# Performance work log

Hardware: AMD Instinct MI355X
Metric: run time of the kernel (lower is better)

## Reference

```python
import jax, jax.numpy as jnp
import numpy as np

N_NODES = 100000
N_EDGES = 3200000
N_FEAT = 128


def setup_inputs() -> dict:
    key = jax.random.key(0)
    ks = jax.random.split(key, 8)
    x = jax.random.normal(ks[0], (N_NODES, N_FEAT), dtype=jnp.float32)
    edge_index = jax.random.randint(ks[1], (2, N_EDGES), 0, N_NODES, dtype=jnp.int64)

    def glorot(k, fan_in, fan_out):
        s = (6.0 / (fan_in + fan_out)) ** 0.5
        return jax.random.uniform(k, (fan_in, fan_out), jnp.float32, -s, s)

    return {
        "x": x,
        "edge_index": edge_index,
        "W1": glorot(ks[2], N_FEAT, 64), "b1": jnp.zeros((64,), jnp.float32),
        "W2": glorot(ks[3], 64, 32),     "b2": jnp.zeros((32,), jnp.float32),
        "W3": glorot(ks[4], 32, 2),      "b3": jnp.zeros((2,), jnp.float32),
    }


def _gcn_norm(edge_index, num_nodes):
    # Add self loops, then symmetric normalization D^{-1/2} (A+I) D^{-1/2}
    loop = jnp.arange(num_nodes, dtype=edge_index.dtype)
    src = jnp.concatenate([edge_index[0], loop])
    dst = jnp.concatenate([edge_index[1], loop])
    deg = jax.ops.segment_sum(jnp.ones_like(dst, dtype=jnp.float32), dst,
                              num_segments=num_nodes)
    dinv = jnp.where(deg > 0, jax.lax.rsqrt(deg), 0.0)
    norm = dinv[src] * dinv[dst]  # [E + N]
    return src, dst, norm


def _gcn_conv(h, W, b, src, dst, norm, num_nodes):
    h = h @ W  # small dense GEMM
    msg = h[src] * norm[:, None]  # gather + scale
    out = jax.ops.segment_sum(msg, dst, num_segments=num_nodes)  # scatter-add
    return out + b


def reference(x, edge_index, W1, b1, W2, b2, W3, b3):
    n = x.shape[0]
    src, dst, norm = _gcn_norm(edge_index, n)
    h = jax.nn.relu(_gcn_conv(x, W1, b1, src, dst, norm, n))
    # dropout(p=0.5) is identity in eval mode
    h = jax.nn.relu(_gcn_conv(h, W2, b2, src, dst, norm, n))
    h = _gcn_conv(h, W3, b3, src, dst, norm, n)
    return jax.nn.log_softmax(h, axis=1)
```

## Files before the change

### kernel.cpp

```cpp
#include <hip/hip_runtime.h>
#include <math.h>

#define EPB 4096
#define CAP 10240

typedef __attribute__((ext_vector_type(8))) short bf16x8;
typedef __attribute__((ext_vector_type(4))) float f32x4;
typedef __attribute__((ext_vector_type(2))) float f32x2;


__device__ inline unsigned short f2b(float f) {
  union { float f; unsigned u; } c; c.f = f;
  unsigned r = c.u + 0x7fff + ((c.u >> 16) & 1);
  return (unsigned short)(r >> 16);
}


__global__ __launch_bounds__(256) void k_bscan2(const int* __restrict__ cnts, int* __restrict__ bbase,
                                                int* __restrict__ rowptr, int E, int N, int NBKT) {
  __shared__ int a[512], c[512];
  int tid = threadIdx.x;
  int v0 = (tid < NBKT) ? cnts[tid] : 0;
  int v1 = (tid + 256 < NBKT) ? cnts[tid + 256] : 0;
  a[tid] = v0; a[tid + 256] = v1;
  __syncthreads();
  int* pin = a; int* pout = c;
  for (int st = 1; st < 512; st <<= 1) {
    pout[tid]       = pin[tid]       + ((tid >= st)       ? pin[tid - st]       : 0);
    pout[tid + 256] = pin[tid + 256] + ((tid + 256 >= st) ? pin[tid + 256 - st] : 0);
    __syncthreads();
    int* t = pin; pin = pout; pout = t;
  }
  if (tid < NBKT)       bbase[tid] = pin[tid] - v0;
  if (tid + 256 < NBKT) bbase[tid + 256] = pin[tid + 256] - v1;
  if (tid == 0) { bbase[NBKT] = E; rowptr[N] = E; }
}


__global__ __launch_bounds__(512) void k_bucket_scatter(const int* __restrict__ src, const int* __restrict__ dst,
                                                        int* __restrict__ gcur, unsigned* __restrict__ tmp,
                                                        int E, int NBKT) {
  __shared__ int hist[512], base[512], loff[512];
  __shared__ int sa[512], sc[512];
  __shared__ unsigned stage[EPB];
  __shared__ unsigned short bkt16[EPB];
  int tid = threadIdx.x;
  int ebeg = blockIdx.x * EPB;
  int eend = min(E, ebeg + EPB);
  hist[tid] = 0;
  __syncthreads();
  int e0 = ebeg + tid * 8;
  int nE = eend - e0; if (nE < 0) nE = 0; if (nE > 8) nE = 8;
  int d[8], s[8], rk[8];
  if (nE == 8) {
#pragma unroll
    for (int q = 0; q < 2; ++q) {
      int4 dv = *(const int4*)(dst + e0 + q * 4);
      int4 sv = *(const int4*)(src + e0 + q * 4);
      d[q * 4 + 0] = dv.x; d[q * 4 + 1] = dv.y; d[q * 4 + 2] = dv.z; d[q * 4 + 3] = dv.w;
      s[q * 4 + 0] = sv.x; s[q * 4 + 1] = sv.y; s[q * 4 + 2] = sv.z; s[q * 4 + 3] = sv.w;
    }
  } else {
#pragma unroll
    for (int k = 0; k < 8; ++k) {
      if (k < nE) { d[k] = dst[e0 + k]; s[k] = src[e0 + k]; } else { d[k] = 0; s[k] = 0; }
    }
  }
#pragma unroll
  for (int k = 0; k < 8; ++k) rk[k] = (k < nE) ? atomicAdd(&hist[d[k] >> 8], 1) : 0;
  __syncthreads();
  int hc = hist[tid];
  sa[tid] = hc;
  base[tid] = (tid < NBKT && hc) ? atomicAdd(&gcur[tid], hc) : 0;
  __syncthreads();
  int* pin = sa; int* pout = sc;
  for (int st = 1; st < 512; st <<= 1) {
    pout[tid] = pin[tid] + ((tid >= st) ? pin[tid - st] : 0);
    __syncthreads();
    int* t = pin; pin = pout; pout = t;
  }
  loff[tid] = pin[tid] - hc;
  __syncthreads();
#pragma unroll
  for (int k = 0; k < 8; ++k) if (k < nE) {
    int bkt = d[k] >> 8;
    int pos = loff[bkt] + rk[k];
    stage[pos] = ((unsigned)s[k] << 8) | (unsigned)(d[k] & 255);
    bkt16[pos] = (unsigned short)bkt;
  }
  __syncthreads();
  int cnt = eend - ebeg;
  for (int k = tid; k < cnt; k += 512) {
    int b = bkt16[k];
    tmp[(size_t)b * CAP + base[b] + (k - loff[b])] = stage[k];
  }
}


__global__ __launch_bounds__(512) void k_bucket_build(const unsigned* __restrict__ tmp, const int* __restrict__ cnts,
                                                      const int* __restrict__ bbase, int* __restrict__ csr,
                                                      int* __restrict__ rowptr, float* __restrict__ dinv, int N) {
  int b = blockIdx.x;
  int tid = threadIdx.x;
  int node0 = b << 8;
  int nn = min(256, N - node0);
  int cnt = cnts[b];
  int gbeg = bbase[b];
  const unsigned* tb = tmp + (size_t)b * CAP;
  __shared__ int h[256], off[256], cur[256];
  __shared__ unsigned short rk[CAP];
  __shared__ int stage[CAP];
  if (tid < 256) h[tid] = 0;
  __syncthreads();
  bool fast = (cnt <= CAP);
  if (fast) {
    for (int e = tid; e < cnt; e += 512) {
      unsigned p = tb[e];
      rk[e] = (unsigned short)atomicAdd(&h[p & 255], 1);
    }
  } else {
    for (int e = tid; e < cnt; e += 512) atomicAdd(&h[tb[e] & 255], 1);
  }
  __syncthreads();
  int deg = 0;
  if (tid < 256) { deg = h[tid]; off[tid] = deg; }
  __syncthreads();
  for (int st = 1; st < 256; st <<= 1) {
    int t = 0;
    if (tid < 256 && tid >= st) t = off[tid - st];
    __syncthreads();
    if (tid < 256) off[tid] += t;
    __syncthreads();
  }
  if (tid < 256) {
    int excl = off[tid] - deg;
    cur[tid] = excl;
    if (tid < nn) {
      rowptr[node0 + tid] = gbeg + excl;
      dinv[node0 + tid] = rsqrtf((float)(deg + 1));
    }
  }
  __syncthreads();
  if (fast) {
    for (int e = tid; e < cnt; e += 512) {
      unsigned p = tb[e];
      stage[cur[p & 255] + (int)rk[e]] = (int)(p >> 8);
    }
    __syncthreads();
    for (int k = tid; k < cnt; k += 512) csr[gbeg + k] = stage[k];
  } else {
    for (int e = tid; e < cnt; e += 512) {
      unsigned p = tb[e];
      int pos = atomicAdd(&cur[p & 255], 1);
      csr[gbeg + pos] = (int)(p >> 8);
    }
  }
}


template <int F_IN, int F_OUT>
__global__ __launch_bounds__(256) void k_gemm_mfma(const float* __restrict__ x, const float* __restrict__ W,
                                                   const float* __restrict__ dinv, unsigned short* __restrict__ g,
                                                   int N, int NT) {
  constexpr int NKS = F_IN / 32;
  constexpr int NCT = F_OUT / 16;
  int tid = threadIdx.x;
  int w = tid >> 6, lane = tid & 63;
  int lo = lane & 15, hi = lane >> 4;

  union U8 { bf16x8 v; unsigned u[4]; };
  U8 bf[NCT][NKS];
#pragma unroll
  for (int ct = 0; ct < NCT; ++ct)
#pragma unroll
    for (int ks = 0; ks < NKS; ++ks) {
      const float* wp = W + (size_t)(ks * 32 + hi * 8) * F_OUT + ct * 16 + lo;
      float f[8];
#pragma unroll
      for (int j = 0; j < 8; ++j) f[j] = wp[(size_t)j * F_OUT];
#pragma unroll
      for (int j = 0; j < 4; ++j)
        asm("v_cvt_pk_bf16_f32 %0, %1, %2" : "=v"(bf[ct][ks].u[j]) : "v"(f[2 * j]), "v"(f[2 * j + 1]));
    }

  for (int t = blockIdx.x * 4 + w; t < NT; t += gridDim.x * 4) {
    int row0 = t << 4;
    f32x4 acc[NCT];
#pragma unroll
    for (int ct = 0; ct < NCT; ++ct) acc[ct] = (f32x4){0.f, 0.f, 0.f, 0.f};
    int rl = row0 + lo; if (rl >= N) rl = N - 1;
    const float* xrow = x + (size_t)rl * F_IN;
#pragma unroll
    for (int ks = 0; ks < NKS; ++ks) {
      const float* xp = xrow + ks * 32 + hi * 8;
      float4 a0 = *(const float4*)xp;
      float4 a1 = *(const float4*)(xp + 4);
      U8 af;
      asm("v_cvt_pk_bf16_f32 %0, %1, %2" : "=v"(af.u[0]) : "v"(a0.x), "v"(a0.y));
      asm("v_cvt_pk_bf16_f32 %0, %1, %2" : "=v"(af.u[1]) : "v"(a0.z), "v"(a0.w));
      asm("v_cvt_pk_bf16_f32 %0, %1, %2" : "=v"(af.u[2]) : "v"(a1.x), "v"(a1.y));
      asm("v_cvt_pk_bf16_f32 %0, %1, %2" : "=v"(af.u[3]) : "v"(a1.z), "v"(a1.w));
#pragma unroll
      for (int ct = 0; ct < NCT; ++ct)
        acc[ct] = __builtin_amdgcn_mfma_f32_16x16x32_bf16(af.v, bf[ct][ks].v, acc[ct], 0, 0, 0);
    }
    float dvv[4];
    if (row0 + 16 <= N) {
      float4 d4 = *(const float4*)(dinv + row0 + (hi << 2));
      dvv[0] = d4.x; dvv[1] = d4.y; dvv[2] = d4.z; dvv[3] = d4.w;
    } else {
#pragma unroll
      for (int j = 0; j < 4; ++j) { int r = row0 + (hi << 2) + j; dvv[j] = dinv[r < N ? r : N - 1]; }
    }
#pragma unroll
    for (int ct = 0; ct < NCT; ++ct) {
#pragma unroll
      for (int j = 0; j < 4; ++j) {
        int row = row0 + (hi << 2) + j;
        if (row < N) g[(size_t)row * F_OUT + ct * 16 + lo] = f2b(dvv[j] * acc[ct][j]);
      }
    }
  }
}


#define ACC2(vv) acc0 += __uint_as_float((vv) << 16); acc1 += __uint_as_float((vv) & 0xffff0000u)

template <int FOUT, bool RELU>
__global__ __launch_bounds__(256) void k_agg_full(const unsigned short* __restrict__ g,
                                                  const int* __restrict__ rowptr, const int* __restrict__ csr,
                                                  const float* __restrict__ dinv, const float* __restrict__ bias,
                                                  float* __restrict__ out, int N) {
  constexpr int LSH = (FOUT == 64) ? 5 : 4;
  constexpr int RSH = (FOUT == 64) ? 7 : 6;
  int t = blockIdx.x * 256 + threadIdx.x;
  int grp = t >> LSH;
  if (grp >= N) return;
  unsigned subB = ((unsigned)t & ((1u << LSH) - 1u)) << 2;
  const char* gb = (const char*)g;
  auto gat = [&](int sid) -> unsigned {
    return *(const unsigned*)(gb + ((((unsigned)sid) << RSH) + subB));
  };
  unsigned u = gat(grp);
  float acc0 = __uint_as_float(u << 16);
  float acc1 = __uint_as_float(u & 0xffff0000u);
  int beg = rowptr[grp], end = rowptr[grp + 1];
  int j = beg;
  for (; j < end && (j & 3); ++j) {
    unsigned v = gat(csr[j]); ACC2(v);
  }
  for (; j + 16 <= end; j += 16) {
    int4 sA = *(const int4*)(csr + j);
    int4 sB = *(const int4*)(csr + j + 4);
    int4 sC = *(const int4*)(csr + j + 8);
    int4 sD = *(const int4*)(csr + j + 12);
    unsigned v0 = gat(sA.x), v1 = gat(sA.y), v2 = gat(sA.z), v3 = gat(sA.w);
    unsigned v4 = gat(sB.x), v5 = gat(sB.y), v6 = gat(sB.z), v7 = gat(sB.w);
    unsigned v8 = gat(sC.x), v9 = gat(sC.y), vA = gat(sC.z), vB = gat(sC.w);
    unsigned vC = gat(sD.x), vD = gat(sD.y), vE = gat(sD.z), vF = gat(sD.w);
    ACC2(v0); ACC2(v1); ACC2(v2); ACC2(v3);
    ACC2(v4); ACC2(v5); ACC2(v6); ACC2(v7);
    ACC2(v8); ACC2(v9); ACC2(vA); ACC2(vB);
    ACC2(vC); ACC2(vD); ACC2(vE); ACC2(vF);
  }
  if (j + 8 <= end) {
    int4 sA = *(const int4*)(csr + j);
    int4 sB = *(const int4*)(csr + j + 4);
    unsigned v0 = gat(sA.x), v1 = gat(sA.y), v2 = gat(sA.z), v3 = gat(sA.w);
    unsigned v4 = gat(sB.x), v5 = gat(sB.y), v6 = gat(sB.z), v7 = gat(sB.w);
    ACC2(v0); ACC2(v1); ACC2(v2); ACC2(v3);
    ACC2(v4); ACC2(v5); ACC2(v6); ACC2(v7);
    j += 8;
  }
  if (j + 4 <= end) {
    int4 sA = *(const int4*)(csr + j);
    unsigned v0 = gat(sA.x), v1 = gat(sA.y), v2 = gat(sA.z), v3 = gat(sA.w);
    ACC2(v0); ACC2(v1); ACC2(v2); ACC2(v3);
    j += 4;
  }
  for (; j < end; ++j) {
    unsigned v = gat(csr[j]); ACC2(v);
  }
  float dv = dinv[grp];
  int fg = (int)(subB >> 1);
  float r0 = fmaf(dv, acc0, bias[fg]);
  float r1 = fmaf(dv, acc1, bias[fg + 1]);
  if (RELU) { r0 = fmaxf(r0, 0.f); r1 = fmaxf(r1, 0.f); }
  *(float2*)(out + (size_t)grp * FOUT + fg) = make_float2(r0, r1);
}


__global__ __launch_bounds__(256) void k_agg2f(const unsigned short* __restrict__ g,
                                               const int* __restrict__ rowptr, const int* __restrict__ csr,
                                               const float* __restrict__ dinv, const float* __restrict__ b2,
                                               const float* __restrict__ W3, unsigned* __restrict__ g2, int N) {
  int t = blockIdx.x * 256 + threadIdx.x;
  int grp = t >> 4;
  if (grp >= N) return;
  unsigned subB = ((unsigned)t & 15u) << 2;
  const char* gb = (const char*)g;
  auto gat = [&](int sid) -> unsigned {
    return *(const unsigned*)(gb + ((((unsigned)sid) << 6) + subB));
  };
  unsigned u = gat(grp);
  float acc0 = __uint_as_float(u << 16);
  float acc1 = __uint_as_float(u & 0xffff0000u);
  int beg = rowptr[grp], end = rowptr[grp + 1];
  int j = beg;
  for (; j < end && (j & 3); ++j) {
    unsigned v = gat(csr[j]); ACC2(v);
  }
  for (; j + 16 <= end; j += 16) {
    int4 sA = *(const int4*)(csr + j);
    int4 sB = *(const int4*)(csr + j + 4);
    int4 sC = *(const int4*)(csr + j + 8);
    int4 sD = *(const int4*)(csr + j + 12);
    unsigned v0 = gat(sA.x), v1 = gat(sA.y), v2 = gat(sA.z), v3 = gat(sA.w);
    unsigned v4 = gat(sB.x), v5 = gat(sB.y), v6 = gat(sB.z), v7 = gat(sB.w);
    unsigned v8 = gat(sC.x), v9 = gat(sC.y), vA = gat(sC.z), vB = gat(sC.w);
    unsigned vC = gat(sD.x), vD = gat(sD.y), vE = gat(sD.z), vF = gat(sD.w);
    ACC2(v0); ACC2(v1); ACC2(v2); ACC2(v3);
    ACC2(v4); ACC2(v5); ACC2(v6); ACC2(v7);
    ACC2(v8); ACC2(v9); ACC2(vA); ACC2(vB);
    ACC2(vC); ACC2(vD); ACC2(vE); ACC2(vF);
  }
  if (j + 8 <= end) {
    int4 sA = *(const int4*)(csr + j);
    int4 sB = *(const int4*)(csr + j + 4);
    unsigned v0 = gat(sA.x), v1 = gat(sA.y), v2 = gat(sA.z), v3 = gat(sA.w);
    unsigned v4 = gat(sB.x), v5 = gat(sB.y), v6 = gat(sB.z), v7 = gat(sB.w);
    ACC2(v0); ACC2(v1); ACC2(v2); ACC2(v3);
    ACC2(v4); ACC2(v5); ACC2(v6); ACC2(v7);
    j += 8;
  }
  if (j + 4 <= end) {
    int4 sA = *(const int4*)(csr + j);
    unsigned v0 = gat(sA.x), v1 = gat(sA.y), v2 = gat(sA.z), v3 = gat(sA.w);
    ACC2(v0); ACC2(v1); ACC2(v2); ACC2(v3);
    j += 4;
  }
  for (; j < end; ++j) {
    unsigned v = gat(csr[j]); ACC2(v);
  }
  float dv = dinv[grp];
  int fg = (int)(subB >> 1);
  float r0 = fmaxf(fmaf(dv, acc0, b2[fg]), 0.f);
  float r1 = fmaxf(fmaf(dv, acc1, b2[fg + 1]), 0.f);
  float4 wv = *(const float4*)(W3 + subB);
  float p0 = r0 * wv.x + r1 * wv.z;
  float p1 = r0 * wv.y + r1 * wv.w;
#pragma unroll
  for (int m = 1; m < 16; m <<= 1) { p0 += __shfl_xor(p0, m); p1 += __shfl_xor(p1, m); }
  if ((t & 15) == 0) {
    unsigned uo = (unsigned)f2b(dv * p0) | ((unsigned)f2b(dv * p1) << 16);
    g2[grp] = uo;
  }
}


__global__ __launch_bounds__(256) void k_final(const unsigned* __restrict__ g2, const int* __restrict__ rowptr,
                                               const int* __restrict__ csr, const float* __restrict__ dinv,
                                               const float* __restrict__ bias, float* __restrict__ out, int N) {
  int i = blockIdx.x * 256 + threadIdx.x;
  if (i >= N) return;
  const char* gb = (const char*)g2;
  unsigned s = *(const unsigned*)(gb + (((unsigned)i) << 2));
  float a0 = __uint_as_float(s << 16), a1 = __uint_as_float(s & 0xffff0000u);
  int beg = rowptr[i], end = rowptr[i + 1];
  int j = beg;
  for (; j < end && (j & 3); ++j) {
    unsigned p = *(const unsigned*)(gb + (((unsigned)csr[j]) << 2));
    a0 += __uint_as_float(p << 16);
    a1 += __uint_as_float(p & 0xffff0000u);
  }
  for (; j + 4 <= end; j += 4) {
    int4 ss = *(const int4*)(csr + j);
    unsigned p0 = *(const unsigned*)(gb + (((unsigned)ss.x) << 2));
    unsigned p1 = *(const unsigned*)(gb + (((unsigned)ss.y) << 2));
    unsigned p2 = *(const unsigned*)(gb + (((unsigned)ss.z) << 2));
    unsigned p3 = *(const unsigned*)(gb + (((unsigned)ss.w) << 2));
    a0 += __uint_as_float(p0 << 16); a1 += __uint_as_float(p0 & 0xffff0000u);
    a0 += __uint_as_float(p1 << 16); a1 += __uint_as_float(p1 & 0xffff0000u);
    a0 += __uint_as_float(p2 << 16); a1 += __uint_as_float(p2 & 0xffff0000u);
    a0 += __uint_as_float(p3 << 16); a1 += __uint_as_float(p3 & 0xffff0000u);
  }
  for (; j < end; ++j) {
    unsigned p = *(const unsigned*)(gb + (((unsigned)csr[j]) << 2));
    a0 += __uint_as_float(p << 16);
    a1 += __uint_as_float(p & 0xffff0000u);
  }
  float dv = dinv[i];
  float v0 = fmaf(dv, a0, bias[0]);
  float v1 = fmaf(dv, a1, bias[1]);
  float m = fmaxf(v0, v1);
  float lse = m + logf(expf(v0 - m) + expf(v1 - m));
  f32x2 o; o.x = v0 - lse; o.y = v1 - lse;
  __builtin_nontemporal_store(o, (f32x2*)(out + 2 * (size_t)i));
}


extern "C" void kernel_launch(void* const* d_in, const int* in_sizes, int n_in,
                              void* d_out, int out_size, void* d_ws, size_t ws_size,
                              hipStream_t stream) {
  const float* x  = (const float*)d_in[0];
  const int*   ei = (const int*)d_in[1];
  const float* W1 = (const float*)d_in[2];
  const float* b1 = (const float*)d_in[3];
  const float* W2 = (const float*)d_in[4];
  const float* b2 = (const float*)d_in[5];
  const float* W3 = (const float*)d_in[6];
  const float* b3 = (const float*)d_in[7];
  float* out = (float*)d_out;

  int N = in_sizes[0] / 128;
  int E = in_sizes[1] / 2;
  const int* src = ei;
  const int* dst = ei + E;
  int NBKT = (N + 255) >> 8;
  int NT = (N + 15) / 16;

  char* w = (char*)d_ws;
  size_t off = 0;
  auto carve = [&](size_t bytes) -> char* {
    char* p = w + off;
    off = (off + bytes + 255) & ~(size_t)255;
    return p;
  };
  float* dinv   = (float*)carve((size_t)N * 4);
  int*   rowptr = (int*)carve((size_t)(N + 1) * 4);
  int*   bbase  = (int*)carve(2048 + 4);
  int*   gcur   = (int*)carve(2048);
  int*   csr    = (int*)carve((size_t)E * 4);
  size_t gsz = (size_t)N * 64 * 2;
  size_t capb = (size_t)NBKT * CAP * 4;
  if (capb > gsz) gsz = capb;
  unsigned short* gbuf = (unsigned short*)carve(gsz);
  float* hbuf   = (float*)carve((size_t)N * 64 * 4);
  unsigned* tmp = (unsigned*)gbuf;
  (void)ws_size; (void)n_in; (void)out_size;

  (void)hipMemsetAsync(gcur, 0, 2048, stream);
  k_bucket_scatter<<<(E + EPB - 1) / EPB, 512, 0, stream>>>(src, dst, gcur, tmp, E, NBKT);
  k_bscan2<<<1, 256, 0, stream>>>(gcur, bbase, rowptr, E, N, NBKT);
  k_bucket_build<<<NBKT, 512, 0, stream>>>(tmp, gcur, bbase, csr, rowptr, dinv, N);

  k_gemm_mfma<128, 64><<<782, 256, 0, stream>>>(x, W1, dinv, gbuf, N, NT);
  k_agg_full<64, true><<<(unsigned)(((long long)N * 32 + 255) / 256), 256, 0, stream>>>(gbuf, rowptr, csr, dinv, b1, hbuf, N);
  k_gemm_mfma<64, 32><<<782, 256, 0, stream>>>(hbuf, W2, dinv, gbuf, N, NT);
  unsigned* g2 = (unsigned*)hbuf;
  k_agg2f<<<(unsigned)(((long long)N * 16 + 255) / 256), 256, 0, stream>>>(gbuf, rowptr, csr, dinv, b2, W3, g2, N);
  k_final<<<(unsigned)((N + 255) / 256), 256, 0, stream>>>(g2, rowptr, csr, dinv, b3, out, N);
}
```

Before: 201.5 us.

## Store layer-1 activations in bf16, fold bucket scan into build, split accumulators

The layer-1 aggregation now writes ReLU output as bf16 instead of fp32, and a new bf16-input MFMA GEMM reads it. This halves the intermediate traffic between aggregation and the second GEMM. The separate single-block bucket prefix-scan kernel is removed: each build block redoes the 512-entry scan in shared memory, which saves a launch but repeats the work in every block. Both aggregation kernels also use two interleaved accumulator pairs to shorten the dependent add chains, and the extra bf16 rounding slightly changes the numerics.

Measured after the change: 199.5 us. About the same (-1.0%).

```diff
diff --git a/kernel.cpp b/kernel.cpp
--- a/kernel.cpp
+++ b/kernel.cpp
@@ -13,27 +13,6 @@
   union { float f; unsigned u; } c; c.f = f;
   unsigned r = c.u + 0x7fff + ((c.u >> 16) & 1);
   return (unsigned short)(r >> 16);
-}
-
-
-__global__ __launch_bounds__(256) void k_bscan2(const int* __restrict__ cnts, int* __restrict__ bbase,
-                                                int* __restrict__ rowptr, int E, int N, int NBKT) {
-  __shared__ int a[512], c[512];
-  int tid = threadIdx.x;
-  int v0 = (tid < NBKT) ? cnts[tid] : 0;
-  int v1 = (tid + 256 < NBKT) ? cnts[tid + 256] : 0;
-  a[tid] = v0; a[tid + 256] = v1;
-  __syncthreads();
-  int* pin = a; int* pout = c;
-  for (int st = 1; st < 512; st <<= 1) {
-    pout[tid]       = pin[tid]       + ((tid >= st)       ? pin[tid - st]       : 0);
-    pout[tid + 256] = pin[tid + 256] + ((tid + 256 >= st) ? pin[tid + 256 - st] : 0);
-    __syncthreads();
-    int* t = pin; pin = pout; pout = t;
-  }
-  if (tid < NBKT)       bbase[tid] = pin[tid] - v0;
-  if (tid + 256 < NBKT) bbase[tid + 256] = pin[tid + 256] - v1;
-  if (tid == 0) { bbase[NBKT] = E; rowptr[N] = E; }
 }
 
 
@@ -98,20 +77,33 @@
 
 
 __global__ __launch_bounds__(512) void k_bucket_build(const unsigned* __restrict__ tmp, const int* __restrict__ cnts,
-                                                      const int* __restrict__ bbase, int* __restrict__ csr,
-                                                      int* __restrict__ rowptr, float* __restrict__ dinv, int N) {
+                                                      int* __restrict__ csr, int* __restrict__ rowptr,
+                                                      float* __restrict__ dinv, int E, int N, int NBKT) {
   int b = blockIdx.x;
   int tid = threadIdx.x;
   int node0 = b << 8;
   int nn = min(256, N - node0);
-  int cnt = cnts[b];
-  int gbeg = bbase[b];
-  const unsigned* tb = tmp + (size_t)b * CAP;
+  __shared__ int sa[512], sc[512];
   __shared__ int h[256], off[256], cur[256];
   __shared__ unsigned short rk[CAP];
   __shared__ int stage[CAP];
+  __shared__ int gbeg_sh;
+  int v = (tid < NBKT) ? cnts[tid] : 0;
+  sa[tid] = v;
   if (tid < 256) h[tid] = 0;
   __syncthreads();
+  int* pin = sa; int* pout = sc;
+  for (int st = 1; st < 512; st <<= 1) {
+    pout[tid] = pin[tid] + ((tid >= st) ? pin[tid - st] : 0);
+    __syncthreads();
+    int* t = pin; pin = pout; pout = t;
+  }
+  if (tid == b) gbeg_sh = pin[tid] - v;
+  if (b == 0 && tid == 0) rowptr[N] = E;
+  __syncthreads();
+  int cnt = cnts[b];
+  int gbeg = gbeg_sh;
+  const unsigned* tb = tmp + (size_t)b * CAP;
   bool fast = (cnt <= CAP);
   if (fast) {
     for (int e = tid; e < cnt; e += 512) {
@@ -224,30 +216,88 @@
 }
 
 
-#define ACC2(vv) acc0 += __uint_as_float((vv) << 16); acc1 += __uint_as_float((vv) & 0xffff0000u)
-
-template <int FOUT, bool RELU>
-__global__ __launch_bounds__(256) void k_agg_full(const unsigned short* __restrict__ g,
-                                                  const int* __restrict__ rowptr, const int* __restrict__ csr,
-                                                  const float* __restrict__ dinv, const float* __restrict__ bias,
-                                                  float* __restrict__ out, int N) {
-  constexpr int LSH = (FOUT == 64) ? 5 : 4;
-  constexpr int RSH = (FOUT == 64) ? 7 : 6;
+template <int F_IN, int F_OUT>
+__global__ __launch_bounds__(256) void k_gemm_mfma_b(const unsigned short* __restrict__ xb, const float* __restrict__ W,
+                                                     const float* __restrict__ dinv, unsigned short* __restrict__ g,
+                                                     int N, int NT) {
+  constexpr int NKS = F_IN / 32;
+  constexpr int NCT = F_OUT / 16;
+  int tid = threadIdx.x;
+  int w = tid >> 6, lane = tid & 63;
+  int lo = lane & 15, hi = lane >> 4;
+
+  union U8 { bf16x8 v; unsigned u[4]; };
+  U8 bf[NCT][NKS];
+#pragma unroll
+  for (int ct = 0; ct < NCT; ++ct)
+#pragma unroll
+    for (int ks = 0; ks < NKS; ++ks) {
+      const float* wp = W + (size_t)(ks * 32 + hi * 8) * F_OUT + ct * 16 + lo;
+      float f[8];
+#pragma unroll
+      for (int j = 0; j < 8; ++j) f[j] = wp[(size_t)j * F_OUT];
+#pragma unroll
+      for (int j = 0; j < 4; ++j)
+        asm("v_cvt_pk_bf16_f32 %0, %1, %2" : "=v"(bf[ct][ks].u[j]) : "v"(f[2 * j]), "v"(f[2 * j + 1]));
+    }
+
+  for (int t = blockIdx.x * 4 + w; t < NT; t += gridDim.x * 4) {
+    int row0 = t << 4;
+    f32x4 acc[NCT];
+#pragma unroll
+    for (int ct = 0; ct < NCT; ++ct) acc[ct] = (f32x4){0.f, 0.f, 0.f, 0.f};
+    int rl = row0 + lo; if (rl >= N) rl = N - 1;
+    const unsigned short* xrow = xb + (size_t)rl * F_IN;
+#pragma unroll
+    for (int ks = 0; ks < NKS; ++ks) {
+      bf16x8 av = *(const bf16x8*)(xrow + ks * 32 + hi * 8);
+#pragma unroll
+      for (int ct = 0; ct < NCT; ++ct)
+        acc[ct] = __builtin_amdgcn_mfma_f32_16x16x32_bf16(av, bf[ct][ks].v, acc[ct], 0, 0, 0);
+    }
+    float dvv[4];
+    if (row0 + 16 <= N) {
+      float4 d4 = *(const float4*)(dinv + row0 + (hi << 2));
+      dvv[0] = d4.x; dvv[1] = d4.y; dvv[2] = d4.z; dvv[3] = d4.w;
+    } else {
+#pragma unroll
+      for (int j = 0; j < 4; ++j) { int r = row0 + (hi << 2) + j; dvv[j] = dinv[r < N ? r : N - 1]; }
+    }
+#pragma unroll
+    for (int ct = 0; ct < NCT; ++ct) {
+#pragma unroll
+      for (int j = 0; j < 4; ++j) {
+        int row = row0 + (hi << 2) + j;
+        if (row < N) g[(size_t)row * F_OUT + ct * 16 + lo] = f2b(dvv[j] * acc[ct][j]);
+      }
+    }
+  }
+}
+
+
+#define ACCa(vv) a0a += __uint_as_float((vv) << 16); a1a += __uint_as_float((vv) & 0xffff0000u)
+#define ACCb(vv) a0b += __uint_as_float((vv) << 16); a1b += __uint_as_float((vv) & 0xffff0000u)
+
+__global__ __launch_bounds__(256) void k_agg1(const unsigned short* __restrict__ g,
+                                              const int* __restrict__ rowptr, const int* __restrict__ csr,
+                                              const float* __restrict__ dinv, const float* __restrict__ bias,
+                                              unsigned short* __restrict__ h1b, int N) {
   int t = blockIdx.x * 256 + threadIdx.x;
-  int grp = t >> LSH;
+  int grp = t >> 5;
   if (grp >= N) return;
-  unsigned subB = ((unsigned)t & ((1u << LSH) - 1u)) << 2;
+  unsigned subB = ((unsigned)t & 31u) << 2;
   const char* gb = (const char*)g;
   auto gat = [&](int sid) -> unsigned {
-    return *(const unsigned*)(gb + ((((unsigned)sid) << RSH) + subB));
+    return *(const unsigned*)(gb + ((((unsigned)sid) << 7) + subB));
   };
   unsigned u = gat(grp);
-  float acc0 = __uint_as_float(u << 16);
-  float acc1 = __uint_as_float(u & 0xffff0000u);
+  float a0a = __uint_as_float(u << 16);
+  float a1a = __uint_as_float(u & 0xffff0000u);
+  float a0b = 0.f, a1b = 0.f;
   int beg = rowptr[grp], end = rowptr[grp + 1];
   int j = beg;
   for (; j < end && (j & 3); ++j) {
-    unsigned v = gat(csr[j]); ACC2(v);
+    unsigned v = gat(csr[j]); ACCa(v);
   }
   for (; j + 16 <= end; j += 16) {
     int4 sA = *(const int4*)(csr + j);
@@ -258,35 +308,36 @@
     unsigned v4 = gat(sB.x), v5 = gat(sB.y), v6 = gat(sB.z), v7 = gat(sB.w);
     unsigned v8 = gat(sC.x), v9 = gat(sC.y), vA = gat(sC.z), vB = gat(sC.w);
     unsigned vC = gat(sD.x), vD = gat(sD.y), vE = gat(sD.z), vF = gat(sD.w);
-    ACC2(v0); ACC2(v1); ACC2(v2); ACC2(v3);
-    ACC2(v4); ACC2(v5); ACC2(v6); ACC2(v7);
-    ACC2(v8); ACC2(v9); ACC2(vA); ACC2(vB);
-    ACC2(vC); ACC2(vD); ACC2(vE); ACC2(vF);
+    ACCa(v0); ACCb(v1); ACCa(v2); ACCb(v3);
+    ACCa(v4); ACCb(v5); ACCa(v6); ACCb(v7);
+    ACCa(v8); ACCb(v9); ACCa(vA); ACCb(vB);
+    ACCa(vC); ACCb(vD); ACCa(vE); ACCb(vF);
   }
   if (j + 8 <= end) {
     int4 sA = *(const int4*)(csr + j);
     int4 sB = *(const int4*)(csr + j + 4);
     unsigned v0 = gat(sA.x), v1 = gat(sA.y), v2 = gat(sA.z), v3 = gat(sA.w);
     unsigned v4 = gat(sB.x), v5 = gat(sB.y), v6 = gat(sB.z), v7 = gat(sB.w);
-    ACC2(v0); ACC2(v1); ACC2(v2); ACC2(v3);
-    ACC2(v4); ACC2(v5); ACC2(v6); ACC2(v7);
+    ACCa(v0); ACCb(v1); ACCa(v2); ACCb(v3);
+    ACCa(v4); ACCb(v5); ACCa(v6); ACCb(v7);
     j += 8;
   }
   if (j + 4 <= end) {
     int4 sA = *(const int4*)(csr + j);
     unsigned v0 = gat(sA.x), v1 = gat(sA.y), v2 = gat(sA.z), v3 = gat(sA.w);
-    ACC2(v0); ACC2(v1); ACC2(v2); ACC2(v3);
+    ACCa(v0); ACCb(v1); ACCa(v2); ACCb(v3);
     j += 4;
   }
   for (; j < end; ++j) {
-    unsigned v = gat(csr[j]); ACC2(v);
-  }
+    unsigned v = gat(csr[j]); ACCa(v);
+  }
+  float acc0 = a0a + a0b, acc1 = a1a + a1b;
   float dv = dinv[grp];
   int fg = (int)(subB >> 1);
-  float r0 = fmaf(dv, acc0, bias[fg]);
-  float r1 = fmaf(dv, acc1, bias[fg + 1]);
-  if (RELU) { r0 = fmaxf(r0, 0.f); r1 = fmaxf(r1, 0.f); }
-  *(float2*)(out + (size_t)grp * FOUT + fg) = make_float2(r0, r1);
+  float r0 = fmaxf(fmaf(dv, acc0, bias[fg]), 0.f);
+  float r1 = fmaxf(fmaf(dv, acc1, bias[fg + 1]), 0.f);
+  unsigned uo = (unsigned)f2b(r0) | ((unsigned)f2b(r1) << 16);
+  *(unsigned*)(h1b + (size_t)grp * 64 + fg) = uo;
 }
 
 
@@ -303,12 +354,13 @@
     return *(const unsigned*)(gb + ((((unsigned)sid) << 6) + subB));
   };
   unsigned u = gat(grp);
-  float acc0 = __uint_as_float(u << 16);
-  float acc1 = __uint_as_float(u & 0xffff0000u);
+  float a0a = __uint_as_float(u << 16);
+  float a1a = __uint_as_float(u & 0xffff0000u);
+  float a0b = 0.f, a1b = 0.f;
   int beg = rowptr[grp], end = rowptr[grp + 1];
   int j = beg;
   for (; j < end && (j & 3); ++j) {
-    unsigned v = gat(csr[j]); ACC2(v);
+    unsigned v = gat(csr[j]); ACCa(v);
   }
   for (; j + 16 <= end; j += 16) {
     int4 sA = *(const int4*)(csr + j);
@@ -319,29 +371,30 @@
     unsigned v4 = gat(sB.x), v5 = gat(sB.y), v6 = gat(sB.z), v7 = gat(sB.w);
     unsigned v8 = gat(sC.x), v9 = gat(sC.y), vA = gat(sC.z), vB = gat(sC.w);
     unsigned vC = gat(sD.x), vD = gat(sD.y), vE = gat(sD.z), vF = gat(sD.w);
-    ACC2(v0); ACC2(v1); ACC2(v2); ACC2(v3);
-    ACC2(v4); ACC2(v5); ACC2(v6); ACC2(v7);
-    ACC2(v8); ACC2(v9); ACC2(vA); ACC2(vB);
-    ACC2(vC); ACC2(vD); ACC2(vE); ACC2(vF);
+    ACCa(v0); ACCb(v1); ACCa(v2); ACCb(v3);
+    ACCa(v4); ACCb(v5); ACCa(v6); ACCb(v7);
+    ACCa(v8); ACCb(v9); ACCa(vA); ACCb(vB);
+    ACCa(vC); ACCb(vD); ACCa(vE); ACCb(vF);
   }
   if (j + 8 <= end) {
     int4 sA = *(const int4*)(csr + j);
     int4 sB = *(const int4*)(csr + j + 4);
     unsigned v0 = gat(sA.x), v1 = gat(sA.y), v2 = gat(sA.z), v3 = gat(sA.w);
     unsigned v4 = gat(sB.x), v5 = gat(sB.y), v6 = gat(sB.z), v7 = gat(sB.w);
-    ACC2(v0); ACC2(v1); ACC2(v2); ACC2(v3);
-    ACC2(v4); ACC2(v5); ACC2(v6); ACC2(v7);
+    ACCa(v0); ACCb(v1); ACCa(v2); ACCb(v3);
+    ACCa(v4); ACCb(v5); ACCa(v6); ACCb(v7);
     j += 8;
   }
   if (j + 4 <= end) {
     int4 sA = *(const int4*)(csr + j);
     unsigned v0 = gat(sA.x), v1 = gat(sA.y), v2 = gat(sA.z), v3 = gat(sA.w);
-    ACC2(v0); ACC2(v1); ACC2(v2); ACC2(v3);
+    ACCa(v0); ACCb(v1); ACCa(v2); ACCb(v3);
     j += 4;
   }
   for (; j < end; ++j) {
-    unsigned v = gat(csr[j]); ACC2(v);
-  }
+    unsigned v = gat(csr[j]); ACCa(v);
+  }
+  float acc0 = a0a + a0b, acc1 = a1a + a1b;
   float dv = dinv[grp];
   int fg = (int)(subB >> 1);
   float r0 = fmaxf(fmaf(dv, acc0, b2[fg]), 0.f);
@@ -428,26 +481,24 @@
   };
   float* dinv   = (float*)carve((size_t)N * 4);
   int*   rowptr = (int*)carve((size_t)(N + 1) * 4);
-  int*   bbase  = (int*)carve(2048 + 4);
   int*   gcur   = (int*)carve(2048);
   int*   csr    = (int*)carve((size_t)E * 4);
   size_t gsz = (size_t)N * 64 * 2;
   size_t capb = (size_t)NBKT * CAP * 4;
   if (capb > gsz) gsz = capb;
   unsigned short* gbuf = (unsigned short*)carve(gsz);
-  float* hbuf   = (float*)carve((size_t)N * 64 * 4);
+  unsigned short* h1b  = (unsigned short*)carve((size_t)N * 64 * 2);
   unsigned* tmp = (unsigned*)gbuf;
   (void)ws_size; (void)n_in; (void)out_size;
 
   (void)hipMemsetAsync(gcur, 0, 2048, stream);
   k_bucket_scatter<<<(E + EPB - 1) / EPB, 512, 0, stream>>>(src, dst, gcur, tmp, E, NBKT);
-  k_bscan2<<<1, 256, 0, stream>>>(gcur, bbase, rowptr, E, N, NBKT);
-  k_bucket_build<<<NBKT, 512, 0, stream>>>(tmp, gcur, bbase, csr, rowptr, dinv, N);
+  k_bucket_build<<<NBKT, 512, 0, stream>>>(tmp, gcur, csr, rowptr, dinv, E, N, NBKT);
 
   k_gemm_mfma<128, 64><<<782, 256, 0, stream>>>(x, W1, dinv, gbuf, N, NT);
-  k_agg_full<64, true><<<(unsigned)(((long long)N * 32 + 255) / 256), 256, 0, stream>>>(gbuf, rowptr, csr, dinv, b1, hbuf, N);
-  k_gemm_mfma<64, 32><<<782, 256, 0, stream>>>(hbuf, W2, dinv, gbuf, N, NT);
-  unsigned* g2 = (unsigned*)hbuf;
+  k_agg1<<<(unsigned)(((long long)N * 32 + 255) / 256), 256, 0, stream>>>(gbuf, rowptr, csr, dinv, b1, h1b, N);
+  k_gemm_mfma_b<64, 32><<<782, 256, 0, stream>>>(h1b, W2, dinv, gbuf, N, NT);
+  unsigned* g2 = (unsigned*)h1b;
   k_agg2f<<<(unsigned)(((long long)N * 16 + 255) / 256), 256, 0, stream>>>(gbuf, rowptr, csr, dinv, b2, W3, g2, N);
   k_final<<<(unsigned)((N + 255) / 256), 256, 0, stream>>>(g2, rowptr, csr, dinv, b3, out, N);
 }
```
